# Kernel optimization log

Measured on AMD Instinct MI355X. Metric: run time of the kernel, lower is better.

Reference implementation:

```python
import jax, jax.numpy as jnp
import numpy as np

N_NODES = 10000
N_EDGES = 160000
D = 512            # input_dim = hidden_size = output_dim
NUM_EXPERTS = 4
N_LAYERS = 2


def setup_inputs() -> dict:
    key = jax.random.key(0)
    k = jax.random.split(key, 7)
    x = jax.random.normal(k[0], (N_NODES, D), dtype=jnp.float32)
    edge_index = jax.random.randint(k[1], (2, N_EDGES), 0, N_NODES, dtype=jnp.int32)
    # Gating network (Linear D -> NUM_EXPERTS)
    gate_w = jax.random.normal(k[2], (D, NUM_EXPERTS), dtype=jnp.float32) * 0.05
    gate_b = jnp.zeros((NUM_EXPERTS,), dtype=jnp.float32)
    # Per-expert SAGEConv weights: lin_r (self/root) and lin_l (neighbor) + bias
    w_self = jax.random.normal(k[3], (NUM_EXPERTS, N_LAYERS, D, D), dtype=jnp.float32) * 0.05
    w_neigh = jax.random.normal(k[4], (NUM_EXPERTS, N_LAYERS, D, D), dtype=jnp.float32) * 0.05
    b_exp = jnp.zeros((NUM_EXPERTS, N_LAYERS, D), dtype=jnp.float32)
    return {"x": x, "edge_index": edge_index, "gate_w": gate_w, "gate_b": gate_b,
            "w_self": w_self, "w_neigh": w_neigh, "b_exp": b_exp, "top_k": 1}


def reference(x, edge_index, gate_w, gate_b, w_self, w_neigh, b_exp, top_k):
    n = x.shape[0]
    src, dst = edge_index[0], edge_index[1]
    # mean-aggregation normalization (PyG SAGEConv aggr='mean'); 0 for isolated nodes
    deg = jax.ops.segment_sum(jnp.ones_like(src, dtype=x.dtype), dst, num_segments=n)
    inv_deg = jnp.where(deg > 0, 1.0 / jnp.maximum(deg, 1.0), 0.0)[:, None]  # [N,1]

    # gating: softmax(Linear(x)) then top-k routing
    gate = jax.nn.softmax(x @ gate_w + gate_b, axis=-1)          # [N, E]
    top_vals, top_idx = jax.lax.top_k(gate, top_k)               # [N, k]

    def expert(ws, wn, b):  # ws, wn: [L, D, D]; b: [L, D]
        h = x
        for l in range(N_LAYERS):
            agg = jax.ops.segment_sum(h[src], dst, num_segments=n) * inv_deg
            # SAGEConv: lin_l(mean_neigh) + lin_r(x) + bias, then relu (norm='id', eval dropout)
            h = jax.nn.relu(agg @ wn[l] + h @ ws[l] + b[l])
        return h

    # dense all-expert compute (matches original module)
    outs = jax.vmap(expert)(w_self, w_neigh, b_exp)              # [E, N, D]
    outs = jnp.transpose(outs, (1, 0, 2))                        # [N, E, D]
    sel = jnp.take_along_axis(outs, top_idx[:, :, None], axis=1)  # [N, k, D]
    return jnp.sum(sel * top_vals[:, :, None], axis=1)           # [N, D]
```

## Files before the change

### kernel.cpp

```cpp
#include <hip/hip_runtime.h>
#include <hip/hip_bf16.h>
#include <cstdint>

#define N_NODES 10000
#define N_EDGES 160000
#define DIM 512
#define K1 1024
#define NEXP 4

typedef __bf16 bf16_t;
typedef bf16_t bf16x8 __attribute__((ext_vector_type(8)));
typedef float f32x4 __attribute__((ext_vector_type(4)));

#define AS1(p) ((__attribute__((address_space(1))) void*)(p))
#define AS3(p) ((__attribute__((address_space(3))) void*)(p))

#define VMW(N) asm volatile("s_waitcnt vmcnt(" #N ")" ::: "memory")
#define MFMA16(d, a_, b_) d = __builtin_amdgcn_mfma_f32_16x16x32_bf16(a_, b_, d, 0, 0, 0)

__global__ void gate_kernel(const float* __restrict__ x,
                            const float* __restrict__ gw,
                            const float* __restrict__ gb,
                            int* __restrict__ top_idx,
                            float* __restrict__ top_val,
                            bf16_t* __restrict__ acat,
                            int* __restrict__ deg,
                            int* __restrict__ ecnt) {
    const int gid = blockIdx.x * 256 + threadIdx.x;
    if (gid < N_NODES) deg[gid] = 0;
    if (gid < NEXP) ecnt[gid] = 0;

    const int wave = threadIdx.x >> 6;
    const int lane = threadIdx.x & 63;
    const int node = blockIdx.x * 4 + wave;
    if (node >= N_NODES) return;
    const float4* x4 = (const float4*)(x + (size_t)node * DIM);
    const float4* gw4 = (const float4*)gw;
    float4 xa = x4[lane * 2];
    float4 xb = x4[lane * 2 + 1];
    float xv[8] = { xa.x, xa.y, xa.z, xa.w, xb.x, xb.y, xb.z, xb.w };
    float a0 = 0.f, a1 = 0.f, a2 = 0.f, a3 = 0.f;
    #pragma unroll
    for (int c = 0; c < 8; c++) {
        float4 g = gw4[lane * 8 + c];
        a0 += xv[c] * g.x; a1 += xv[c] * g.y; a2 += xv[c] * g.z; a3 += xv[c] * g.w;
    }
    bf16x8 o;
    #pragma unroll
    for (int c = 0; c < 8; c++) o[c] = (bf16_t)xv[c];
    *(bf16x8*)(acat + (size_t)node * K1 + DIM + lane * 8) = o;
    for (int off = 32; off > 0; off >>= 1) {
        a0 += __shfl_xor(a0, off);
        a1 += __shfl_xor(a1, off);
        a2 += __shfl_xor(a2, off);
        a3 += __shfl_xor(a3, off);
    }
    if (lane == 0) {
        float z[4] = { a0 + gb[0], a1 + gb[1], a2 + gb[2], a3 + gb[3] };
        int bi = 0; float bm = z[0];
        for (int e = 1; e < 4; e++) if (z[e] > bm) { bm = z[e]; bi = e; }
        float den = 0.f;
        for (int e = 0; e < 4; e++) den += expf(z[e] - bm);
        top_idx[node] = bi;
        top_val[node] = 1.0f / den;
    }
}

__global__ void bucket_kernel(const int* __restrict__ top_idx,
                              int* __restrict__ ecnt,
                              int* __restrict__ lists) {
    __shared__ int lcnt[NEXP];
    __shared__ int base[NEXP];
    const int tid = threadIdx.x;
    if (tid < NEXP) lcnt[tid] = 0;
    __syncthreads();
    const int node = blockIdx.x * 256 + tid;
    int e = 0, rank = 0;
    if (node < N_NODES) {
        e = top_idx[node];
        rank = atomicAdd(&lcnt[e], 1);
    }
    __syncthreads();
    if (tid < NEXP) base[tid] = atomicAdd(&ecnt[tid], lcnt[tid]);
    __syncthreads();
    if (node < N_NODES) lists[e * N_NODES + base[e] + rank] = node;
}

__global__ void deg_kernel(const int* __restrict__ dst, int* __restrict__ deg) {
    int i = blockIdx.x * blockDim.x + threadIdx.x;
    if (i < N_EDGES) atomicAdd(&deg[dst[i]], 1);
}

__global__ void scan_kernel(const int* __restrict__ deg,
                            int* __restrict__ offs,
                            int* __restrict__ cursor,
                            const int* __restrict__ ecnt,
                            int* __restrict__ jobs) {
    __shared__ int wsum[16];
    __shared__ int carrysh;
    const int tid = threadIdx.x;
    const int lane = tid & 63;
    const int wv = tid >> 6;
    if (tid == 0) {
        carrysh = 0;
        int pref = 0;
        for (int e2 = 0; e2 < NEXP; e2++) {
            jobs[e2] = pref;
            pref += (ecnt[e2] + 127) >> 7;
        }
        jobs[4] = pref;
    }
    __syncthreads();
    for (int base = 0; base < N_NODES; base += 1024) {
        int i = base + tid;
        int v = (i < N_NODES) ? deg[i] : 0;
        int s = v;
        #pragma unroll
        for (int off = 1; off < 64; off <<= 1) {
            int t = __shfl_up(s, off);
            if (lane >= off) s += t;
        }
        if (lane == 63) wsum[wv] = s;
        int carry = carrysh;
        __syncthreads();
        if (wv == 0) {
            int w = (lane < 16) ? wsum[lane] : 0;
            #pragma unroll
            for (int off = 1; off < 16; off <<= 1) {
                int t = __shfl_up(w, off);
                if (lane >= off) w += t;
            }
            if (lane < 16) wsum[lane] = w;
        }
        __syncthreads();
        int wbase = (wv > 0) ? wsum[wv - 1] : 0;
        int excl = carry + wbase + s - v;
        if (i < N_NODES) { offs[i] = excl; cursor[i] = excl; }
        int total = wsum[15];
        __syncthreads();
        if (tid == 0) carrysh = carry + total;
        __syncthreads();
    }
    if (tid == 0) offs[N_NODES] = carrysh;
}

__global__ void fill_kernel(const int* __restrict__ src, const int* __restrict__ dst,
                            int* __restrict__ cursor, int* __restrict__ csr) {
    int i = blockIdx.x * blockDim.x + threadIdx.x;
    if (i < N_EDGES) {
        int d = dst[i];
        int p = atomicAdd(&cursor[d], 1);
        csr[p] = src[i];
    }
}

__global__ void wtrans_kernel(const float* __restrict__ w_neigh,
                              const float* __restrict__ w_self,
                              bf16_t* __restrict__ Bt) {
    __shared__ float tile[32][33];
    const int m = blockIdx.z;
    const bool isSelf = m >= 8;
    const int el = m & 7;
    const float* W = (isSelf ? w_self : w_neigh) + (size_t)el * DIM * DIM;
    const int k0 = blockIdx.x * 32;
    const int n0 = blockIdx.y * 32;
    const int tx = threadIdx.x, ty = threadIdx.y;
    for (int r = ty; r < 32; r += 8)
        tile[r][tx] = W[(size_t)(k0 + r) * DIM + n0 + tx];
    __syncthreads();
    for (int r = ty; r < 32; r += 8) {
        int n = n0 + r;
        int k = k0 + tx;
        Bt[((size_t)el * DIM + n) * K1 + (isSelf ? DIM : 0) + k] = (bf16_t)tile[tx][r];
    }
}

__global__ void agg1_kernel(const int* __restrict__ offs, const int* __restrict__ csr,
                            bf16_t* __restrict__ acat) {
    const int wave = threadIdx.x >> 6;
    const int lane = threadIdx.x & 63;
    const int node = blockIdx.x * 4 + wave;
    if (node >= N_NODES) return;
    const int c0 = lane * 8;
    float s[8] = {0,0,0,0,0,0,0,0};
    int beg = offs[node];
    int end = offs[node + 1];
    int d = end - beg;
    int p = beg;
    for (; p + 8 <= end; p += 8) {
        bf16x8 v[8];
        #pragma unroll
        for (int q = 0; q < 8; q++) {
            int idx = csr[p + q];
            v[q] = *(const bf16x8*)(acat + (size_t)idx * K1 + DIM + c0);
        }
        #pragma unroll
        for (int q = 0; q < 8; q++)
            #pragma unroll
            for (int k = 0; k < 8; k++) s[k] += (float)v[q][k];
    }
    for (; p + 4 <= end; p += 4) {
        bf16x8 v[4];
        #pragma unroll
        for (int q = 0; q < 4; q++) {
            int idx = csr[p + q];
            v[q] = *(const bf16x8*)(acat + (size_t)idx * K1 + DIM + c0);
        }
        #pragma unroll
        for (int q = 0; q < 4; q++)
            #pragma unroll
            for (int k = 0; k < 8; k++) s[k] += (float)v[q][k];
    }
    for (; p < end; p++) {
        int idx = csr[p];
        bf16x8 v0 = *(const bf16x8*)(acat + (size_t)idx * K1 + DIM + c0);
        #pragma unroll
        for (int k = 0; k < 8; k++) s[k] += (float)v0[k];
    }
    float w = d > 0 ? 1.0f / (float)d : 0.0f;
    bf16x8 o;
    #pragma unroll
    for (int k = 0; k < 8; k++) o[k] = (bf16_t)(s[k] * w);
    *(bf16x8*)(acat + (size_t)node * K1 + c0) = o;
}

__global__ void agg2_kernel(const int* __restrict__ offs, const int* __restrict__ csr,
                            const int* __restrict__ top_idx,
                            const bf16_t* __restrict__ h1, bf16_t* __restrict__ acat) {
    const int wave = threadIdx.x >> 6;
    const int lane = threadIdx.x & 63;
    const int node = blockIdx.x * 4 + wave;
    if (node >= N_NODES) return;
    const int c0 = lane * 8;
    const bf16_t* hb = h1 + (size_t)top_idx[node] * N_NODES * DIM;
    float s[8] = {0,0,0,0,0,0,0,0};
    int beg = offs[node];
    int end = offs[node + 1];
    int d = end - beg;
    int p = beg;
    for (; p + 8 <= end; p += 8) {
        bf16x8 v[8];
        #pragma unroll
        for (int q = 0; q < 8; q++) {
            int idx = csr[p + q];
            v[q] = *(const bf16x8*)(hb + (size_t)idx * DIM + c0);
        }
        #pragma unroll
        for (int q = 0; q < 8; q++)
            #pragma unroll
            for (int k = 0; k < 8; k++) s[k] += (float)v[q][k];
    }
    for (; p + 4 <= end; p += 4) {
        bf16x8 v[4];
        #pragma unroll
        for (int q = 0; q < 4; q++) {
            int idx = csr[p + q];
            v[q] = *(const bf16x8*)(hb + (size_t)idx * DIM + c0);
        }
        #pragma unroll
        for (int q = 0; q < 4; q++)
            #pragma unroll
            for (int k = 0; k < 8; k++) s[k] += (float)v[q][k];
    }
    for (; p < end; p++) {
        int idx = csr[p];
        bf16x8 v0 = *(const bf16x8*)(hb + (size_t)idx * DIM + c0);
        #pragma unroll
        for (int k = 0; k < 8; k++) s[k] += (float)v0[k];
    }
    float w = d > 0 ? 1.0f / (float)d : 0.0f;
    bf16x8 o;
    #pragma unroll
    for (int k = 0; k < 8; k++) o[k] = (bf16_t)(s[k] * w);
    *(bf16x8*)(acat + (size_t)node * K1 + c0) = o;
    *(bf16x8*)(acat + (size_t)node * K1 + DIM + c0) = *(const bf16x8*)(hb + (size_t)node * DIM + c0);
}

__global__ __launch_bounds__(512, 2)
void gemm_l1_kernel(const bf16_t* __restrict__ A,
                    const bf16_t* __restrict__ Bt,
                    const float* __restrict__ bias_all,
                    bf16_t* __restrict__ h1) {
    const int b = blockIdx.x;
    const int xcd = b & 7;
    const int loc = b >> 3;
    const int mtile = xcd * 2 + (loc >> 4);
    const int ntile = loc & 15;
    const int e = ntile >> 2;

    __shared__ __align__(16) bf16_t As[3 * 640 * 32];
    __shared__ __align__(16) bf16_t Bs[3 * 128 * 32];

    const int t = threadIdx.x;
    const int lane = t & 63;
    const int wave = t >> 6;
    const int rloc = t >> 2;
    const int cgl = ((t & 3) - ((t >> 3) & 3)) & 3;

    const bf16_t* pA0 = A + (size_t)min(mtile * 640 +   0 + rloc, N_NODES - 1) * K1 + cgl * 8;
    const bf16_t* pA1 = A + (size_t)min(mtile * 640 + 128 + rloc, N_NODES - 1) * K1 + cgl * 8;
    const bf16_t* pA2 = A + (size_t)min(mtile * 640 + 256 + rloc, N_NODES - 1) * K1 + cgl * 8;
    const bf16_t* pA3 = A + (size_t)min(mtile * 640 + 384 + rloc, N_NODES - 1) * K1 + cgl * 8;
    const bf16_t* pA4 = A + (size_t)min(mtile * 640 + 512 + rloc, N_NODES - 1) * K1 + cgl * 8;
    const bf16_t* pB0 = Bt + ((size_t)(e * 2 + 0) * DIM + (ntile & 3) * 128 + rloc) * K1 + cgl * 8;

    char* asb = (char*)&As[0];
    char* bsb = (char*)&Bs[0];

    auto stage_full = [&](int bu) {
        char* ab = asb + bu * 40960 + wave * 1024;
        char* bb = bsb + bu * 8192  + wave * 1024;
        __builtin_amdgcn_global_load_lds(AS1(pA0), AS3(ab),          16, 0, 0);
        __builtin_amdgcn_global_load_lds(AS1(pA1), AS3(ab + 8192),   16, 0, 0);
        __builtin_amdgcn_global_load_lds(AS1(pA2), AS3(ab + 16384),  16, 0, 0);
        __builtin_amdgcn_global_load_lds(AS1(pA3), AS3(ab + 24576),  16, 0, 0);
        __builtin_amdgcn_global_load_lds(AS1(pA4), AS3(ab + 32768),  16, 0, 0);
        __builtin_amdgcn_global_load_lds(AS1(pB0), AS3(bb),          16, 0, 0);
        pA0 += 32; pA1 += 32; pA2 += 32; pA3 += 32; pA4 += 32; pB0 += 32;
    };

    const int rfr = lane & 15;
    const int cpr = lane >> 4;
    const int wm = wave >> 1;
    const int wn = wave & 1;
    const int arow = wm * 160 + rfr;
    const int brow = wn * 64 + rfr;
    const int ppA = (cpr + (arow >> 1)) & 3;
    const int ppB = (cpr + (brow >> 1)) & 3;
    const int aoff = arow * 32 + ppA * 8;
    const int boff = brow * 32 + ppB * 8;

    f32x4 acc[10][4] = {};

    auto compute_full = [&](int bu) {
        const bf16_t* Ab = As + bu * 20480 + aoff;
        const bf16_t* Bb = Bs + bu * 4096  + boff;
        bf16x8 bfr[4];
        #pragma unroll
        for (int j = 0; j < 4; j++) bfr[j] = *(const bf16x8*)(Bb + j * 512);
        #pragma unroll
        for (int i = 0; i < 10; i++) {
            bf16x8 af = *(const bf16x8*)(Ab + i * 512);
            #pragma unroll
            for (int j = 0; j < 4; j++)
                MFMA16(acc[i][j], af, bfr[j]);
        }
    };

    stage_full(0);
    stage_full(1);

    int cb = 0, sb = 2;
    for (int tt = 0; tt < 31; ++tt) {
        VMW(6);
        __builtin_amdgcn_s_barrier();
        asm volatile("" ::: "memory");
        const bool st = (tt < 30);
        char* ab = asb + sb * 40960 + wave * 1024;
        char* bb = bsb + sb * 8192  + wave * 1024;
        const bf16_t* Ab = As + cb * 20480 + aoff;
        const bf16_t* Bb = Bs + cb * 4096  + boff;

        bf16x8 bq[4], aq[4];

        #pragma unroll
        for (int j = 0; j < 4; j++) bq[j] = *(const bf16x8*)(Bb + j * 512);
        #pragma unroll
        for (int i = 0; i < 4; i++) aq[i] = *(const bf16x8*)(Ab + i * 512);
        if (st) {
            __builtin_amdgcn_global_load_lds(AS1(pA0), AS3(ab),        16, 0, 0);
            __builtin_amdgcn_global_load_lds(AS1(pA1), AS3(ab + 8192), 16, 0, 0);
        }
        __builtin_amdgcn_s_barrier();
        asm volatile("s_waitcnt lgkmcnt(0)" ::: "memory");
        __builtin_amdgcn_sched_barrier(0);
        __builtin_amdgcn_s_setprio(1);
        #pragma unroll
        for (int i = 0; i < 4; i++)
            #pragma unroll
            for (int j = 0; j < 4; j++)
                MFMA16(acc[i][j], aq[i], bq[j]);
        __builtin_amdgcn_s_setprio(0);

        #pragma unroll
        for (int i = 0; i < 3; i++) aq[i] = *(const bf16x8*)(Ab + (4 + i) * 512);
        if (st) {
            __builtin_amdgcn_global_load_lds(AS1(pA2), AS3(ab + 16384), 16, 0, 0);
            __builtin_amdgcn_global_load_lds(AS1(pA3), AS3(ab + 24576), 16, 0, 0);
        }
        __builtin_amdgcn_s_barrier();
        asm volatile("s_waitcnt lgkmcnt(0)" ::: "memory");
        __builtin_amdgcn_sched_barrier(0);
        __builtin_amdgcn_s_setprio(1);
        #pragma unroll
        for (int i = 0; i < 3; i++)
            #pragma unroll
            for (int j = 0; j < 4; j++)
                MFMA16(acc[4 + i][j], aq[i], bq[j]);
        __builtin_amdgcn_s_setprio(0);

        #pragma unroll
        for (int i = 0; i < 3; i++) aq[i] = *(const bf16x8*)(Ab + (7 + i) * 512);
        if (st) {
            __builtin_amdgcn_global_load_lds(AS1(pA4), AS3(ab + 32768), 16, 0, 0);
            __builtin_amdgcn_global_load_lds(AS1(pB0), AS3(bb),         16, 0, 0);
        }
        __builtin_amdgcn_s_barrier();
        asm volatile("s_waitcnt lgkmcnt(0)" ::: "memory");
        __builtin_amdgcn_sched_barrier(0);
        __builtin_amdgcn_s_setprio(1);
        #pragma unroll
        for (int i = 0; i < 3; i++)
            #pragma unroll
            for (int j = 0; j < 4; j++)
                MFMA16(acc[7 + i][j], aq[i], bq[j]);
        __builtin_amdgcn_s_setprio(0);

        if (st) {
            pA0 += 32; pA1 += 32; pA2 += 32; pA3 += 32; pA4 += 32; pB0 += 32;
            sb = (sb == 2) ? 0 : sb + 1;
        }
        cb = (cb == 2) ? 0 : cb + 1;
    }
    VMW(0);
    __builtin_amdgcn_s_barrier();
    asm volatile("" ::: "memory");
    compute_full(cb);

    const float* bias = bias_all + e * 1024;
    const int cobase = (ntile & 3) * 128 + wn * 64 + (lane & 15);
    float bv[4];
    #pragma unroll
    for (int j = 0; j < 4; j++) bv[j] = bias[cobase + j * 16];
    const int rbase = mtile * 640 + wm * 160 + (lane >> 4) * 4;
    #pragma unroll
    for (int i = 0; i < 10; i++) {
        #pragma unroll
        for (int r = 0; r < 4; r++) {
            int row = rbase + i * 16 + r;
            if (row < N_NODES) {
                bf16_t* cp = h1 + ((size_t)e * N_NODES + row) * DIM + cobase;
                #pragma unroll
                for (int j = 0; j < 4; j++) {
                    float v = fmaxf(acc[i][j][r] + bv[j], 0.f);
                    cp[j * 16] = (bf16_t)v;
                }
            }
        }
    }
}

__global__ __launch_bounds__(256)
void gemm2_kernel(const bf16_t* __restrict__ A,
                  const bf16_t* __restrict__ Bt,
                  const float* __restrict__ bias_all,
                  float* __restrict__ out,
                  const int* __restrict__ lists,
                  const int* __restrict__ ecnt,
                  const int* __restrict__ jobs,
                  const float* __restrict__ top_val) {
    __shared__ __align__(16) bf16_t As[3 * 128 * 32];
    __shared__ __align__(16) bf16_t Bs[3 * 128 * 32];

    const int t = threadIdx.x;
    const int lane = t & 63;
    const int wave = t >> 6;
    const int wm = wave >> 1;
    const int wn = wave & 1;
    const int r0 = t >> 2;
    const int rot = (t >> 3) & 3;
    const int cgl = ((t & 3) - rot) & 3;
    const int cpr = lane >> 4;
    const int rfr = lane & 15;
    char* asb = (char*)&As[0];
    char* bsb = (char*)&Bs[0];
    const int wb = wave * 1024;

    const int total = jobs[4] * 4;

    for (int j = blockIdx.x; j < total; j += gridDim.x) {
        const int byt = j >> 2;
        const int bx = j & 3;
        const int e = (byt >= jobs[1]) + (byt >= jobs[2]) + (byt >= jobs[3]);
        const int by = byt - jobs[e];
        const int cnt = ecnt[e];
        const int cmax = max(cnt, 1);

        int i0 = by * 128 + r0;
        int i1 = i0 + 64;
        int arow0 = lists[e * N_NODES + min(i0, cmax - 1)];
        int arow1 = lists[e * N_NODES + min(i1, cmax - 1)];
        arow0 = min(max(arow0, 0), N_NODES - 1);
        arow1 = min(max(arow1, 0), N_NODES - 1);
        const bf16_t* Bte = Bt + (size_t)(e * 2 + 1) * DIM * K1;
        const bf16_t* aptr0 = A + (size_t)arow0 * K1 + cgl * 8;
        const bf16_t* aptr1 = A + (size_t)arow1 * K1 + cgl * 8;
        const bf16_t* bptr0 = Bte + (size_t)(bx * 128 + r0) * K1 + cgl * 8;
        const bf16_t* bptr1 = bptr0 + (size_t)64 * K1;

        f32x4 acc[4][4] = {};

        auto stage = [&](int bu) {
            char* ab = asb + bu * 8192 + wb;
            char* bb = bsb + bu * 8192 + wb;
            __builtin_amdgcn_global_load_lds(AS1(aptr0), AS3(ab),        16, 0, 0);
            __builtin_amdgcn_global_load_lds(AS1(aptr1), AS3(ab + 4096), 16, 0, 0);
            __builtin_amdgcn_global_load_lds(AS1(bptr0), AS3(bb),        16, 0, 0);
            __builtin_amdgcn_global_load_lds(AS1(bptr1), AS3(bb + 4096), 16, 0, 0);
            aptr0 += 32; aptr1 += 32; bptr0 += 32; bptr1 += 32;
        };

        auto compute = [&](int bu) {
            const bf16_t* Ab = As + bu * 4096;
            const bf16_t* Bb = Bs + bu * 4096;
            bf16x8 af[4], bfr[4];
            #pragma unroll
            for (int i = 0; i < 4; i++) {
                int r_full = wm * 64 + i * 16 + rfr;
                int p = (cpr + (r_full >> 1)) & 3;
                af[i] = *(const bf16x8*)(Ab + r_full * 32 + p * 8);
            }
            #pragma unroll
            for (int jj = 0; jj < 4; jj++) {
                int r_full = wn * 64 + jj * 16 + rfr;
                int p = (cpr + (r_full >> 1)) & 3;
                bfr[jj] = *(const bf16x8*)(Bb + r_full * 32 + p * 8);
            }
            #pragma unroll
            for (int i = 0; i < 4; i++)
                #pragma unroll
                for (int jj = 0; jj < 4; jj++)
                    MFMA16(acc[i][jj], af[i], bfr[jj]);
        };

        __builtin_amdgcn_s_barrier();
        asm volatile("" ::: "memory");

        stage(0);
        stage(1);
        int cb = 0, sb = 2;
        for (int tt = 0; tt < 31; ++tt) {
            VMW(4);
            __builtin_amdgcn_s_barrier();
            asm volatile("" ::: "memory");
            if (tt < 30) {
                stage(sb);
                sb = (sb == 2) ? 0 : sb + 1;
            }
            compute(cb);
            cb = (cb == 2) ? 0 : cb + 1;
        }
        VMW(0);
        __builtin_amdgcn_s_barrier();
        asm volatile("" ::: "memory");
        compute(cb);

        const float* bias = bias_all + e * 1024 + DIM;
        const int cbase = bx * 128 + wn * 64 + (lane & 15);
        float bv[4];
        #pragma unroll
        for (int jj = 0; jj < 4; jj++) bv[jj] = bias[cbase + jj * 16];
        #pragma unroll
        for (int i = 0; i < 4; i++) {
            #pragma unroll
            for (int r = 0; r < 4; r++) {
                int row = by * 128 + wm * 64 + i * 16 + (lane >> 4) * 4 + r;
                if (row < cnt) {
                    int node = lists[e * N_NODES + row];
                    float tv = top_val[node];
                    float* cp = out + (size_t)node * DIM + cbase;
                    #pragma unroll
                    for (int jj = 0; jj < 4; jj++) {
                        float v = fmaxf(acc[i][jj][r] + bv[jj], 0.f);
                        cp[jj * 16] = v * tv;
                    }
                }
            }
        }
    }
}

extern "C" void kernel_launch(void* const* d_in, const int* in_sizes, int n_in,
                              void* d_out, int out_size, void* d_ws, size_t ws_size,
                              hipStream_t stream) {
    const float* x       = (const float*)d_in[0];
    const int*   edge    = (const int*)d_in[1];
    const float* gw      = (const float*)d_in[2];
    const float* gb      = (const float*)d_in[3];
    const float* w_self  = (const float*)d_in[4];
    const float* w_neigh = (const float*)d_in[5];
    const float* b_exp   = (const float*)d_in[6];
    float* out = (float*)d_out;

    char* p = (char*)d_ws;
    auto alloc = [&](size_t bytes) {
        char* r = p;
        p += (bytes + 255) & ~(size_t)255;
        return r;
    };
    bf16_t* Bt      = (bf16_t*)alloc((size_t)8 * DIM * K1 * 2);
    bf16_t* acat    = (bf16_t*)alloc((size_t)N_NODES * K1 * 2);
    bf16_t* h1      = (bf16_t*)alloc((size_t)NEXP * N_NODES * DIM * 2);
    int*    deg     = (int*)alloc((size_t)N_NODES * 4);
    int*    offs    = (int*)alloc((size_t)(N_NODES + 1) * 4);
    int*    cursor  = (int*)alloc((size_t)N_NODES * 4);
    int*    csr     = (int*)alloc((size_t)N_EDGES * 4);
    int*    top_idx = (int*)alloc((size_t)N_NODES * 4);
    float*  top_val = (float*)alloc((size_t)N_NODES * 4);
    int*    ecnt    = (int*)alloc(256);
    int*    lists   = (int*)alloc((size_t)NEXP * N_NODES * 4);
    int*    jobs    = ecnt + 8;

    const int* srcE = edge;
    const int* dstE = edge + N_EDGES;

    gate_kernel<<<N_NODES / 4, 256, 0, stream>>>(x, gw, gb, top_idx, top_val, acat, deg, ecnt);
    bucket_kernel<<<40, 256, 0, stream>>>(top_idx, ecnt, lists);
    deg_kernel<<<N_EDGES / 256, 256, 0, stream>>>(dstE, deg);
    scan_kernel<<<1, 1024, 0, stream>>>(deg, offs, cursor, ecnt, jobs);
    fill_kernel<<<N_EDGES / 256, 256, 0, stream>>>(srcE, dstE, cursor, csr);
    wtrans_kernel<<<dim3(16, 16, 16), dim3(32, 8), 0, stream>>>(w_neigh, w_self, Bt);
    agg1_kernel<<<N_NODES / 4, 256, 0, stream>>>(offs, csr, acat);
    gemm_l1_kernel<<<256, 512, 0, stream>>>(acat, Bt, b_exp, h1);
    agg2_kernel<<<N_NODES / 4, 256, 0, stream>>>(offs, csr, top_idx, h1, acat);
    gemm2_kernel<<<320, 256, 0, stream>>>(acat, Bt, b_exp, out, lists, ecnt, jobs, top_val);
}
```

Measured before the change: 268.8 us.

## Merge small setup kernels and retile layer-1 GEMM to smaller double-buffered blocks

Folds the bucket and degree kernels into one launch, and the CSR fill and weight transpose into another, cutting launch overhead and serial gaps. The layer-1 GEMM now uses 256-thread blocks with 320-row M tiles across 512 blocks. The LDS ring drops from triple to double buffering, and the loop waits on all loads each iteration. This adds parallelism and occupancy but gives up some load/compute overlap and B-tile reuse per block.

```diff
diff --git a/kernel.cpp b/kernel.cpp
--- a/kernel.cpp
+++ b/kernel.cpp
@@ -66,29 +66,31 @@
     }
 }
 
-__global__ void bucket_kernel(const int* __restrict__ top_idx,
-                              int* __restrict__ ecnt,
-                              int* __restrict__ lists) {
-    __shared__ int lcnt[NEXP];
-    __shared__ int base[NEXP];
-    const int tid = threadIdx.x;
-    if (tid < NEXP) lcnt[tid] = 0;
-    __syncthreads();
-    const int node = blockIdx.x * 256 + tid;
-    int e = 0, rank = 0;
-    if (node < N_NODES) {
-        e = top_idx[node];
-        rank = atomicAdd(&lcnt[e], 1);
-    }
-    __syncthreads();
-    if (tid < NEXP) base[tid] = atomicAdd(&ecnt[tid], lcnt[tid]);
-    __syncthreads();
-    if (node < N_NODES) lists[e * N_NODES + base[e] + rank] = node;
-}
-
-__global__ void deg_kernel(const int* __restrict__ dst, int* __restrict__ deg) {
-    int i = blockIdx.x * blockDim.x + threadIdx.x;
-    if (i < N_EDGES) atomicAdd(&deg[dst[i]], 1);
+__global__ void bucket_deg_kernel(const int* __restrict__ top_idx,
+                                  int* __restrict__ ecnt,
+                                  int* __restrict__ lists,
+                                  const int* __restrict__ dst,
+                                  int* __restrict__ deg) {
+    const int gi = blockIdx.x * 256 + threadIdx.x;
+    if (gi < N_EDGES) atomicAdd(&deg[dst[gi]], 1);
+
+    if (blockIdx.x < 40) {
+        __shared__ int lcnt[NEXP];
+        __shared__ int base[NEXP];
+        const int tid = threadIdx.x;
+        if (tid < NEXP) lcnt[tid] = 0;
+        __syncthreads();
+        const int node = blockIdx.x * 256 + tid;
+        int e = 0, rank = 0;
+        if (node < N_NODES) {
+            e = top_idx[node];
+            rank = atomicAdd(&lcnt[e], 1);
+        }
+        __syncthreads();
+        if (tid < NEXP) base[tid] = atomicAdd(&ecnt[tid], lcnt[tid]);
+        __syncthreads();
+        if (node < N_NODES) lists[e * N_NODES + base[e] + rank] = node;
+    }
 }
 
 __global__ void scan_kernel(const int* __restrict__ deg,
@@ -144,34 +146,36 @@
     if (tid == 0) offs[N_NODES] = carrysh;
 }
 
-__global__ void fill_kernel(const int* __restrict__ src, const int* __restrict__ dst,
-                            int* __restrict__ cursor, int* __restrict__ csr) {
-    int i = blockIdx.x * blockDim.x + threadIdx.x;
-    if (i < N_EDGES) {
-        int d = dst[i];
-        int p = atomicAdd(&cursor[d], 1);
-        csr[p] = src[i];
-    }
-}
-
-__global__ void wtrans_kernel(const float* __restrict__ w_neigh,
-                              const float* __restrict__ w_self,
-                              bf16_t* __restrict__ Bt) {
-    __shared__ float tile[32][33];
-    const int m = blockIdx.z;
-    const bool isSelf = m >= 8;
-    const int el = m & 7;
-    const float* W = (isSelf ? w_self : w_neigh) + (size_t)el * DIM * DIM;
-    const int k0 = blockIdx.x * 32;
-    const int n0 = blockIdx.y * 32;
-    const int tx = threadIdx.x, ty = threadIdx.y;
-    for (int r = ty; r < 32; r += 8)
-        tile[r][tx] = W[(size_t)(k0 + r) * DIM + n0 + tx];
-    __syncthreads();
-    for (int r = ty; r < 32; r += 8) {
-        int n = n0 + r;
-        int k = k0 + tx;
-        Bt[((size_t)el * DIM + n) * K1 + (isSelf ? DIM : 0) + k] = (bf16_t)tile[tx][r];
+__global__ void fill_wtrans_kernel(const int* __restrict__ src, const int* __restrict__ dst,
+                                   int* __restrict__ cursor, int* __restrict__ csr,
+                                   const float* __restrict__ w_neigh,
+                                   const float* __restrict__ w_self,
+                                   bf16_t* __restrict__ Bt) {
+    if (blockIdx.x < 625) {
+        int i = blockIdx.x * 256 + threadIdx.x;
+        if (i < N_EDGES) {
+            int d = dst[i];
+            int p = atomicAdd(&cursor[d], 1);
+            csr[p] = src[i];
+        }
+    } else {
+        __shared__ float tile[32][33];
+        const int q = blockIdx.x - 625;
+        const int m = q >> 8;
+        const bool isSelf = m >= 8;
+        const int el = m & 7;
+        const float* W = (isSelf ? w_self : w_neigh) + (size_t)el * DIM * DIM;
+        const int k0 = (q & 15) * 32;
+        const int n0 = ((q >> 4) & 15) * 32;
+        const int tx = threadIdx.x & 31, ty = threadIdx.x >> 5;
+        for (int r = ty; r < 32; r += 8)
+            tile[r][tx] = W[(size_t)(k0 + r) * DIM + n0 + tx];
+        __syncthreads();
+        for (int r = ty; r < 32; r += 8) {
+            int n = n0 + r;
+            int k = k0 + tx;
+            Bt[((size_t)el * DIM + n) * K1 + (isSelf ? DIM : 0) + k] = (bf16_t)tile[tx][r];
+        }
     }
 }
 
@@ -276,7 +280,7 @@
     *(bf16x8*)(acat + (size_t)node * K1 + DIM + c0) = *(const bf16x8*)(hb + (size_t)node * DIM + c0);
 }
 
-__global__ __launch_bounds__(512, 2)
+__global__ __launch_bounds__(256, 2)
 void gemm_l1_kernel(const bf16_t* __restrict__ A,
                     const bf16_t* __restrict__ Bt,
                     const float* __restrict__ bias_all,
@@ -284,12 +288,12 @@
     const int b = blockIdx.x;
     const int xcd = b & 7;
     const int loc = b >> 3;
-    const int mtile = xcd * 2 + (loc >> 4);
+    const int mtile = xcd * 4 + (loc >> 4);
     const int ntile = loc & 15;
     const int e = ntile >> 2;
 
-    __shared__ __align__(16) bf16_t As[3 * 640 * 32];
-    __shared__ __align__(16) bf16_t Bs[3 * 128 * 32];
+    __shared__ __align__(16) bf16_t As[2 * 320 * 32];
+    __shared__ __align__(16) bf16_t Bs[2 * 128 * 32];
 
     const int t = threadIdx.x;
     const int lane = t & 63;
@@ -297,27 +301,16 @@
     const int rloc = t >> 2;
     const int cgl = ((t & 3) - ((t >> 3) & 3)) & 3;
 
-    const bf16_t* pA0 = A + (size_t)min(mtile * 640 +   0 + rloc, N_NODES - 1) * K1 + cgl * 8;
-    const bf16_t* pA1 = A + (size_t)min(mtile * 640 + 128 + rloc, N_NODES - 1) * K1 + cgl * 8;
-    const bf16_t* pA2 = A + (size_t)min(mtile * 640 + 256 + rloc, N_NODES - 1) * K1 + cgl * 8;
-    const bf16_t* pA3 = A + (size_t)min(mtile * 640 + 384 + rloc, N_NODES - 1) * K1 + cgl * 8;
-    const bf16_t* pA4 = A + (size_t)min(mtile * 640 + 512 + rloc, N_NODES - 1) * K1 + cgl * 8;
+    const bf16_t* pA0 = A + (size_t)min(mtile * 320 +   0 + rloc, N_NODES - 1) * K1 + cgl * 8;
+    const bf16_t* pA1 = A + (size_t)min(mtile * 320 +  64 + rloc, N_NODES - 1) * K1 + cgl * 8;
+    const bf16_t* pA2 = A + (size_t)min(mtile * 320 + 128 + rloc, N_NODES - 1) * K1 + cgl * 8;
+    const bf16_t* pA3 = A + (size_t)min(mtile * 320 + 192 + rloc, N_NODES - 1) * K1 + cgl * 8;
+    const bf16_t* pA4 = A + (size_t)min(mtile * 320 + 256 + rloc, N_NODES - 1) * K1 + cgl * 8;
     const bf16_t* pB0 = Bt + ((size_t)(e * 2 + 0) * DIM + (ntile & 3) * 128 + rloc) * K1 + cgl * 8;
+    const bf16_t* pB1 = pB0 + (size_t)64 * K1;
 
     char* asb = (char*)&As[0];
     char* bsb = (char*)&Bs[0];
-
-    auto stage_full = [&](int bu) {
-        char* ab = asb + bu * 40960 + wave * 1024;
-        char* bb = bsb + bu * 8192  + wave * 1024;
-        __builtin_amdgcn_global_load_lds(AS1(pA0), AS3(ab),          16, 0, 0);
-        __builtin_amdgcn_global_load_lds(AS1(pA1), AS3(ab + 8192),   16, 0, 0);
-        __builtin_amdgcn_global_load_lds(AS1(pA2), AS3(ab + 16384),  16, 0, 0);
-        __builtin_amdgcn_global_load_lds(AS1(pA3), AS3(ab + 24576),  16, 0, 0);
-        __builtin_amdgcn_global_load_lds(AS1(pA4), AS3(ab + 32768),  16, 0, 0);
-        __builtin_amdgcn_global_load_lds(AS1(pB0), AS3(bb),          16, 0, 0);
-        pA0 += 32; pA1 += 32; pA2 += 32; pA3 += 32; pA4 += 32; pB0 += 32;
-    };
 
     const int rfr = lane & 15;
     const int cpr = lane >> 4;
@@ -332,34 +325,30 @@
 
     f32x4 acc[10][4] = {};
 
-    auto compute_full = [&](int bu) {
-        const bf16_t* Ab = As + bu * 20480 + aoff;
-        const bf16_t* Bb = Bs + bu * 4096  + boff;
-        bf16x8 bfr[4];
-        #pragma unroll
-        for (int j = 0; j < 4; j++) bfr[j] = *(const bf16x8*)(Bb + j * 512);
-        #pragma unroll
-        for (int i = 0; i < 10; i++) {
-            bf16x8 af = *(const bf16x8*)(Ab + i * 512);
-            #pragma unroll
-            for (int j = 0; j < 4; j++)
-                MFMA16(acc[i][j], af, bfr[j]);
-        }
-    };
-
-    stage_full(0);
-    stage_full(1);
-
-    int cb = 0, sb = 2;
-    for (int tt = 0; tt < 31; ++tt) {
-        VMW(6);
+    {
+        char* ab = asb + wave * 1024;
+        char* bb = bsb + wave * 1024;
+        __builtin_amdgcn_global_load_lds(AS1(pA0), AS3(ab),          16, 0, 0);
+        __builtin_amdgcn_global_load_lds(AS1(pA1), AS3(ab + 4096),   16, 0, 0);
+        __builtin_amdgcn_global_load_lds(AS1(pA2), AS3(ab + 8192),   16, 0, 0);
+        __builtin_amdgcn_global_load_lds(AS1(pA3), AS3(ab + 12288),  16, 0, 0);
+        __builtin_amdgcn_global_load_lds(AS1(pA4), AS3(ab + 16384),  16, 0, 0);
+        __builtin_amdgcn_global_load_lds(AS1(pB0), AS3(bb),          16, 0, 0);
+        __builtin_amdgcn_global_load_lds(AS1(pB1), AS3(bb + 4096),   16, 0, 0);
+        pA0 += 32; pA1 += 32; pA2 += 32; pA3 += 32; pA4 += 32; pB0 += 32; pB1 += 32;
+    }
+
+    for (int tt = 0; tt < 32; ++tt) {
+        VMW(0);
         __builtin_amdgcn_s_barrier();
         asm volatile("" ::: "memory");
-        const bool st = (tt < 30);
-        char* ab = asb + sb * 40960 + wave * 1024;
-        char* bb = bsb + sb * 8192  + wave * 1024;
-        const bf16_t* Ab = As + cb * 20480 + aoff;
-        const bf16_t* Bb = Bs + cb * 4096  + boff;
+        const bool st = (tt < 31);
+        const int sbu = (tt + 1) & 1;
+        const int cbu = tt & 1;
+        char* ab = asb + sbu * 20480 + wave * 1024;
+        char* bb = bsb + sbu * 8192  + wave * 1024;
+        const bf16_t* Ab = As + cbu * 10240 + aoff;
+        const bf16_t* Bb = Bs + cbu * 4096  + boff;
 
         bf16x8 bq[4], aq[4];
 
@@ -369,7 +358,8 @@
         for (int i = 0; i < 4; i++) aq[i] = *(const bf16x8*)(Ab + i * 512);
         if (st) {
             __builtin_amdgcn_global_load_lds(AS1(pA0), AS3(ab),        16, 0, 0);
-            __builtin_amdgcn_global_load_lds(AS1(pA1), AS3(ab + 8192), 16, 0, 0);
+            __builtin_amdgcn_global_load_lds(AS1(pA1), AS3(ab + 4096), 16, 0, 0);
+            __builtin_amdgcn_global_load_lds(AS1(pA2), AS3(ab + 8192), 16, 0, 0);
         }
         __builtin_amdgcn_s_barrier();
         asm volatile("s_waitcnt lgkmcnt(0)" ::: "memory");
@@ -385,8 +375,8 @@
         #pragma unroll
         for (int i = 0; i < 3; i++) aq[i] = *(const bf16x8*)(Ab + (4 + i) * 512);
         if (st) {
-            __builtin_amdgcn_global_load_lds(AS1(pA2), AS3(ab + 16384), 16, 0, 0);
-            __builtin_amdgcn_global_load_lds(AS1(pA3), AS3(ab + 24576), 16, 0, 0);
+            __builtin_amdgcn_global_load_lds(AS1(pA3), AS3(ab + 12288), 16, 0, 0);
+            __builtin_amdgcn_global_load_lds(AS1(pA4), AS3(ab + 16384), 16, 0, 0);
         }
         __builtin_amdgcn_s_barrier();
         asm volatile("s_waitcnt lgkmcnt(0)" ::: "memory");
@@ -402,8 +392,8 @@
         #pragma unroll
         for (int i = 0; i < 3; i++) aq[i] = *(const bf16x8*)(Ab + (7 + i) * 512);
         if (st) {
-            __builtin_amdgcn_global_load_lds(AS1(pA4), AS3(ab + 32768), 16, 0, 0);
-            __builtin_amdgcn_global_load_lds(AS1(pB0), AS3(bb),         16, 0, 0);
+            __builtin_amdgcn_global_load_lds(AS1(pB0), AS3(bb),        16, 0, 0);
+            __builtin_amdgcn_global_load_lds(AS1(pB1), AS3(bb + 4096), 16, 0, 0);
         }
         __builtin_amdgcn_s_barrier();
         asm volatile("s_waitcnt lgkmcnt(0)" ::: "memory");
@@ -417,22 +407,16 @@
         __builtin_amdgcn_s_setprio(0);
 
         if (st) {
-            pA0 += 32; pA1 += 32; pA2 += 32; pA3 += 32; pA4 += 32; pB0 += 32;
-            sb = (sb == 2) ? 0 : sb + 1;
-        }
-        cb = (cb == 2) ? 0 : cb + 1;
-    }
-    VMW(0);
-    __builtin_amdgcn_s_barrier();
-    asm volatile("" ::: "memory");
-    compute_full(cb);
+            pA0 += 32; pA1 += 32; pA2 += 32; pA3 += 32; pA4 += 32; pB0 += 32; pB1 += 32;
+        }
+    }
 
     const float* bias = bias_all + e * 1024;
     const int cobase = (ntile & 3) * 128 + wn * 64 + (lane & 15);
     float bv[4];
     #pragma unroll
     for (int j = 0; j < 4; j++) bv[j] = bias[cobase + j * 16];
-    const int rbase = mtile * 640 + wm * 160 + (lane >> 4) * 4;
+    const int rbase = mtile * 320 + wm * 160 + (lane >> 4) * 4;
     #pragma unroll
     for (int i = 0; i < 10; i++) {
         #pragma unroll
@@ -615,13 +599,11 @@
     const int* dstE = edge + N_EDGES;
 
     gate_kernel<<<N_NODES / 4, 256, 0, stream>>>(x, gw, gb, top_idx, top_val, acat, deg, ecnt);
-    bucket_kernel<<<40, 256, 0, stream>>>(top_idx, ecnt, lists);
-    deg_kernel<<<N_EDGES / 256, 256, 0, stream>>>(dstE, deg);
+    bucket_deg_kernel<<<N_EDGES / 256, 256, 0, stream>>>(top_idx, ecnt, lists, dstE, deg);
     scan_kernel<<<1, 1024, 0, stream>>>(deg, offs, cursor, ecnt, jobs);
-    fill_kernel<<<N_EDGES / 256, 256, 0, stream>>>(srcE, dstE, cursor, csr);
-    wtrans_kernel<<<dim3(16, 16, 16), dim3(32, 8), 0, stream>>>(w_neigh, w_self, Bt);
+    fill_wtrans_kernel<<<625 + 4096, 256, 0, stream>>>(srcE, dstE, cursor, csr, w_neigh, w_self, Bt);
     agg1_kernel<<<N_NODES / 4, 256, 0, stream>>>(offs, csr, acat);
-    gemm_l1_kernel<<<256, 512, 0, stream>>>(acat, Bt, b_exp, h1);
+    gemm_l1_kernel<<<512, 256, 0, stream>>>(acat, Bt, b_exp, h1);
     agg2_kernel<<<N_NODES / 4, 256, 0, stream>>>(offs, csr, top_idx, h1, acat);
     gemm2_kernel<<<320, 256, 0, stream>>>(acat, Bt, b_exp, out, lists, ecnt, jobs, top_val);
 }
```

Measured after the change: 263.8 us. No clear change (-1.9%).
